# Performance work log

Measured on AMD Instinct MI355X. Metric: run time of the kernel, lower is better.

Reference implementation:

```python
import jax, jax.numpy as jnp
import numpy as np

B, C, H, W = 8, 64, 64, 64
CQ = C // 8  # query/key channels


def setup_inputs() -> dict:
    key = jax.random.key(0)
    ks = jax.random.split(key, 7)
    s = 0.05
    return {
        "x": jax.random.normal(ks[0], (B, C, H, W), jnp.float32),
        "wq": jax.random.normal(ks[1], (CQ, C), jnp.float32) * s,
        "bq": jnp.zeros((CQ,), jnp.float32),
        "wk": jax.random.normal(ks[2], (CQ, C), jnp.float32) * s,
        "bk": jnp.zeros((CQ,), jnp.float32),
        "wv": jax.random.normal(ks[3], (C, C), jnp.float32) * s,
        "bv": jnp.zeros((C,), jnp.float32),
    }


def reference(x, wq, bq, wk, bk, wv, bv):
    b, c, h, w = x.shape
    n = h * w
    xf = x.reshape(b, c, n)                       # [B, C, N]
    # 1x1 convs == per-pixel linear over channels
    q = jnp.einsum('oc,bcn->bon', wq, xf) + bq[None, :, None]   # [B, CQ, N]
    k = jnp.einsum('oc,bcn->bon', wk, xf) + bk[None, :, None]   # [B, CQ, N]
    v = jnp.einsum('oc,bcn->bon', wv, xf) + bv[None, :, None]   # [B, C, N]
    # energy[b, i, j] = q[b, :, i] . k[b, :, j]  (unscaled)
    energy = jnp.einsum('bci,bcj->bij', q, k)     # [B, N, N]
    attention = jax.nn.softmax(energy, axis=-1)   # softmax over j
    # out[b, c, i] = sum_j v[b, c, j] * attention[b, i, j]
    out = jnp.einsum('bcj,bij->bci', v, attention)
    return out.reshape(b, c, h, w)
```

## Files before the change

### kernel.cpp

```cpp
#include <hip/hip_runtime.h>
#include <hip/hip_bf16.h>


#define B_   8
#define C_   64
#define N_   4096
#define LOG2E 1.44269504088896340736f

typedef short bf16x8 __attribute__((ext_vector_type(8)));
typedef float f32x4  __attribute__((ext_vector_type(4)));
typedef unsigned int uint32;

#if __has_builtin(__builtin_amdgcn_exp2f)
#define EXP2(x) __builtin_amdgcn_exp2f(x)
#else
#define EXP2(x) __expf((x) * 0.69314718055994530942f)
#endif

__device__ __forceinline__ unsigned short f2bf_rn(float f) {
    union { __hip_bfloat16 h; unsigned short u; } cv;
    cv.h = __float2bfloat16(f);
    return cv.u;
}
__device__ __forceinline__ uint32 pk_rn(float lo, float hi) {
    return (uint32)f2bf_rn(lo) | ((uint32)f2bf_rn(hi) << 16);
}
__device__ __forceinline__ uint32 pack_rtz(float lo, float hi) {
    return __builtin_amdgcn_perm(__float_as_uint(hi), __float_as_uint(lo), 0x07060302);
}

__global__ __launch_bounds__(256) void prep_kernel(
    const float* __restrict__ x,
    const float* __restrict__ wq, const float* __restrict__ bq,
    const float* __restrict__ wk, const float* __restrict__ bk,
    unsigned short* __restrict__ Qh, unsigned short* __restrict__ Kh,
    unsigned short* __restrict__ Xb)
{
    __shared__ float Xs[C_][64];
    __shared__ float Wqk[16][C_];
    __shared__ float Bqk[16];

    const int t  = threadIdx.x;
    const int b  = blockIdx.x >> 6;
    const int p0 = (blockIdx.x & 63) << 6;

    for (int i = t; i < 1024; i += 256) {
        int o = i >> 6;
        Wqk[o][i & 63] = (o < 8) ? wq[i] * LOG2E : wk[i - 512];
    }
    if (t < 16) Bqk[t] = (t < 8) ? bq[t] * LOG2E : bk[t - 8];

    for (int i = t; i < 2048; i += 256) {
        int c = i >> 5, p2 = (i & 31) << 1;
        const float* xp = x + ((size_t)b * C_ + c) * N_ + p0 + p2;
        float2 v = *(const float2*)xp;
        Xs[c][p2] = v.x; Xs[c][p2 + 1] = v.y;
        *(uint32*)(Xb + ((size_t)b * C_ + c) * N_ + p0 + p2) = pk_rn(v.x, v.y);
    }
    __syncthreads();

    const int pix = t & 63, grp = t >> 6;
    float a[4];
    #pragma unroll
    for (int r = 0; r < 4; ++r) a[r] = Bqk[grp * 4 + r];
    for (int c = 0; c < C_; ++c) {
        float xv = Xs[c][pix];
        #pragma unroll
        for (int r = 0; r < 4; ++r) a[r] += Wqk[grp * 4 + r][c] * xv;
    }
    #pragma unroll
    for (int r = 0; r < 4; ++r) {
        int o = grp * 4 + r;
        unsigned short hv = f2bf_rn(a[r]);
        if (o < 8) Qh[((size_t)b * N_ + p0 + pix) * 8 + o] = hv;
        else       Kh[((size_t)b * N_ + p0 + pix) * 8 + (o - 8)] = hv;
    }
}

__global__ __launch_bounds__(256) void attn_mfma3_kernel(
    const unsigned short* __restrict__ Qh,
    const unsigned short* __restrict__ Kh,
    const unsigned short* __restrict__ Xb,
    const float* __restrict__ wv, const float* __restrict__ bv,
    float* __restrict__ out)
{
    __shared__ __align__(16) char smem[66560];

    const int t    = threadIdx.x;
    const int w    = t >> 6;
    const int lane = t & 63;
    const int l16  = lane & 15;
    const int qd   = lane >> 4;
    const int b    = blockIdx.x >> 6;
    const int i0   = (blockIdx.x & 63) << 6;

    const bf16x8 z8 = {};
    const f32x4  zf = {};

    bf16x8 qf[4];
    #pragma unroll
    for (int qt = 0; qt < 4; ++qt) {
        qf[qt] = z8;
        if (qd == 0)
            qf[qt] = *(const bf16x8*)(Qh + ((size_t)b * N_ + i0 + qt * 16 + l16) * 8);
    }

    const unsigned short* Kp = Kh + ((size_t)b * N_ + w * 1024) * 8;
    const unsigned short* Xp = Xb + (size_t)b * C_ * N_ + w * 1024;

    f32x4 acc[4][4];
    #pragma unroll
    for (int ct = 0; ct < 4; ++ct)
        #pragma unroll
        for (int qt = 0; qt < 4; ++qt) acc[ct][qt] = zf;
    float dsum[4] = {0.f, 0.f, 0.f, 0.f};

    const int swz   = (l16 & 3) << 2;
    const int wbase = w * 4096 + l16 * 64;
    int woff[2];
    #pragma unroll
    for (int jt = 0; jt < 2; ++jt) woff[jt] = ((jt * 8 + qd * 2) ^ swz) << 2;
    const int roff = ((qd * 4) ^ swz) << 2;

    bf16x8 kf[2][2], xf[2][4];
    #pragma unroll
    for (int jt = 0; jt < 2; ++jt) {
        kf[0][jt] = z8;
        if (qd == 0) kf[0][jt] = *(const bf16x8*)(Kp + (jt * 16 + l16) * 8);
    }
    #pragma unroll
    for (int ct = 0; ct < 4; ++ct)
        xf[0][ct] = *(const bf16x8*)(Xp + (size_t)(ct * 16 + l16) * N_ + qd * 8);

    #pragma unroll 2
    for (int s = 0; s < 32; ++s) {
        const int cur = s & 1, nxt = cur ^ 1;
        const int jb = s * 32;

        f32x4 sf[2][4];
        #pragma unroll
        for (int jt = 0; jt < 2; ++jt)
            #pragma unroll
            for (int qt = 0; qt < 4; ++qt)
                sf[jt][qt] = __builtin_amdgcn_mfma_f32_16x16x32_bf16(kf[cur][jt], qf[qt], zf, 0, 0, 0);

        if (s < 31) {
            #pragma unroll
            for (int jt = 0; jt < 2; ++jt) {
                bf16x8 nk = z8;
                if (qd == 0) nk = *(const bf16x8*)(Kp + (size_t)(jb + 32 + jt * 16 + l16) * 8);
                kf[nxt][jt] = nk;
            }
            #pragma unroll
            for (int ct = 0; ct < 4; ++ct)
                xf[nxt][ct] = *(const bf16x8*)(Xp + (size_t)(ct * 16 + l16) * N_ + jb + 32 + qd * 8);
        }

        #pragma unroll
        for (int jt = 0; jt < 2; ++jt)
            #pragma unroll
            for (int qt = 0; qt < 4; ++qt) {
                float e0 = EXP2(sf[jt][qt][0]);
                float e1 = EXP2(sf[jt][qt][1]);
                float e2 = EXP2(sf[jt][qt][2]);
                float e3 = EXP2(sf[jt][qt][3]);
                dsum[qt] += (e0 + e1) + (e2 + e3);
                uint2 u;
                u.x = pack_rtz(e0, e1);
                u.y = pack_rtz(e2, e3);
                *(uint2*)(smem + wbase + qt * 1024 + woff[jt]) = u;
            }

        #pragma unroll
        for (int qt = 0; qt < 4; ++qt) {
            bf16x8 pb = *(const bf16x8*)(smem + wbase + qt * 1024 + roff);
            #pragma unroll
            for (int ct = 0; ct < 4; ++ct)
                acc[ct][qt] = __builtin_amdgcn_mfma_f32_16x16x32_bf16(xf[cur][ct], pb, acc[ct][qt], 0, 0, 0);
        }
    }

    #pragma unroll
    for (int qt = 0; qt < 4; ++qt) {
        float v = dsum[qt];
        v += __shfl_xor(v, 16, 64);
        v += __shfl_xor(v, 32, 64);
        if (qd == 0) *(float*)(smem + 65536 + (w * 64 + qt * 16 + l16) * 4) = v;
    }
    if (w > 0) {
        char* rb = smem + 16384 + (w - 1) * 16384;
        #pragma unroll
        for (int ct = 0; ct < 4; ++ct)
            #pragma unroll
            for (int qt = 0; qt < 4; ++qt)
                *(f32x4*)(rb + (ct * 4 + qt) * 1024 + lane * 16) = acc[ct][qt];
    }
    __syncthreads();

    if (w == 0) {
        #pragma unroll
        for (int rr = 0; rr < 3; ++rr)
            #pragma unroll
            for (int ct = 0; ct < 4; ++ct)
                #pragma unroll
                for (int qt = 0; qt < 4; ++qt) {
                    f32x4 p = *(const f32x4*)(smem + 16384 + rr * 16384 + (ct * 4 + qt) * 1024 + lane * 16);
                    acc[ct][qt] += p;
                }
        float* Or = (float*)(smem + 16384);
        #pragma unroll
        for (int ct = 0; ct < 4; ++ct)
            #pragma unroll
            for (int qt = 0; qt < 4; ++qt)
                #pragma unroll
                for (int r = 0; r < 4; ++r)
                    Or[(ct * 16 + qd * 4 + r) * 64 + qt * 16 + l16] = acc[ct][qt][r];
    } else {
        float* Wvs = (float*)smem;
        for (int i = t - 64; i < 4096; i += 192) Wvs[i] = wv[i];
    }
    __syncthreads();

    const int q = t & 63, grp = t >> 6;
    const float* Wvs = (const float*)smem;
    const float* Or  = (const float*)(smem + 16384);
    const float* Dn  = (const float*)(smem + 65536);
    const float inv = 1.0f / (Dn[q] + Dn[64 + q] + Dn[128 + q] + Dn[192 + q]);
    float o[16];
    #pragma unroll
    for (int r = 0; r < 16; ++r) o[r] = 0.f;
    for (int k = 0; k < 64; ++k) {
        float ov = Or[k * 64 + q];
        #pragma unroll
        for (int r = 0; r < 16; ++r)
            o[r] += Wvs[(grp * 16 + r) * 64 + k] * ov;
    }
    #pragma unroll
    for (int r = 0; r < 16; ++r)
        out[((size_t)b * C_ + grp * 16 + r) * N_ + i0 + q] = o[r] * inv + bv[grp * 16 + r];
}

__global__ __launch_bounds__(256) void attn_fused_fallback(
    const float* __restrict__ x,
    const float* __restrict__ wq, const float* __restrict__ bq,
    const float* __restrict__ wk, const float* __restrict__ bk,
    const float* __restrict__ wv, const float* __restrict__ bv,
    float* __restrict__ out)
{
    __shared__ float Qs[64][8];
    __shared__ float Ks[8][64];
    __shared__ float Vs[64][C_];
    __shared__ float Ws[64][64 + 1];
    __shared__ float Xs[C_ * 64];
    __shared__ float Wks[8][C_];
    __shared__ float Wvs[C_][C_ + 1];

    const int t     = threadIdx.x;
    const int b     = blockIdx.x / (N_ / 64);
    const int i0    = (blockIdx.x % (N_ / 64)) * 64;
    const int jlane = t & 63;
    const int wgrp  = t >> 6;

    for (int l = t; l < 8 * C_;  l += 256) Wks[l >> 6][l & 63] = wk[l];
    for (int l = t; l < C_ * C_; l += 256) Wvs[l >> 6][l & 63] = wv[l];
    for (int l = t; l < C_ * 64; l += 256)
        Xs[(l >> 6) * 64 + (l & 63)] = x[((size_t)b * C_ + (l >> 6)) * N_ + i0 + (l & 63)];
    __syncthreads();
    {
        int qi = jlane;
        #pragma unroll
        for (int r = 0; r < 2; ++r) {
            int cc = wgrp * 2 + r;
            float a = bq[cc];
            for (int c = 0; c < C_; ++c) a += wq[cc * C_ + c] * Xs[c * 64 + qi];
            Qs[qi][cc] = a;
        }
    }
    __syncthreads();

    const int qi2 = t >> 2;
    const int cb  = (t & 3) << 4;
    float accv[16];
    #pragma unroll
    for (int r = 0; r < 16; ++r) accv[r] = 0.f;
    float denom = 0.f;

    for (int j0 = 0; j0 < N_; j0 += 64) {
        for (int l = t; l < C_ * 64; l += 256)
            Xs[(l >> 6) * 64 + (l & 63)] = x[((size_t)b * C_ + (l >> 6)) * N_ + j0 + (l & 63)];
        __syncthreads();
        {
            int j = jlane;
            #pragma unroll
            for (int r = 0; r < 2; ++r) {
                int cc = wgrp * 2 + r;
                float a = bk[cc];
                for (int c = 0; c < C_; ++c) a += Wks[cc][c] * Xs[c * 64 + j];
                Ks[cc][j] = a;
            }
        }
        {
            int vc = jlane;
            #pragma unroll 2
            for (int r = 0; r < 16; ++r) {
                int j = wgrp * 16 + r;
                float a = bv[vc];
                for (int c = 0; c < C_; ++c) a += Wvs[vc][c] * Xs[c * 64 + j];
                Vs[j][vc] = a;
            }
        }
        __syncthreads();
        {
            float kreg[8];
            #pragma unroll
            for (int cc = 0; cc < 8; ++cc) kreg[cc] = Ks[cc][jlane];
            #pragma unroll 4
            for (int r = 0; r < 16; ++r) {
                int qi = wgrp * 16 + r;
                float e = 0.f;
                #pragma unroll
                for (int cc = 0; cc < 8; ++cc) e += Qs[qi][cc] * kreg[cc];
                Ws[qi][jlane] = __expf(e);
            }
        }
        __syncthreads();
        #pragma unroll 4
        for (int j = 0; j < 64; ++j) {
            float wv2 = Ws[qi2][j];
            denom += wv2;
            const float4* vrow = (const float4*)(&Vs[j][cb]);
            float4 v0 = vrow[0], v1 = vrow[1], v2 = vrow[2], v3 = vrow[3];
            accv[0]  += wv2 * v0.x; accv[1]  += wv2 * v0.y; accv[2]  += wv2 * v0.z; accv[3]  += wv2 * v0.w;
            accv[4]  += wv2 * v1.x; accv[5]  += wv2 * v1.y; accv[6]  += wv2 * v1.z; accv[7]  += wv2 * v1.w;
            accv[8]  += wv2 * v2.x; accv[9]  += wv2 * v2.y; accv[10] += wv2 * v2.z; accv[11] += wv2 * v2.w;
            accv[12] += wv2 * v3.x; accv[13] += wv2 * v3.y; accv[14] += wv2 * v3.z; accv[15] += wv2 * v3.w;
        }
        __syncthreads();
    }

    const float inv = 1.0f / denom;
    #pragma unroll
    for (int r = 0; r < 16; ++r)
        out[((size_t)b * C_ + cb + r) * N_ + i0 + qi2] = accv[r] * inv;
}

extern "C" void kernel_launch(void* const* d_in, const int* in_sizes, int n_in,
                              void* d_out, int out_size, void* d_ws, size_t ws_size,
                              hipStream_t stream)
{
    const float* x  = (const float*)d_in[0];
    const float* wq = (const float*)d_in[1];
    const float* bq = (const float*)d_in[2];
    const float* wk = (const float*)d_in[3];
    const float* bk = (const float*)d_in[4];
    const float* wv = (const float*)d_in[5];
    const float* bv = (const float*)d_in[6];
    float* out = (float*)d_out;

    const size_t nQ = (size_t)B_ * N_ * 8;
    const size_t nX = (size_t)B_ * C_ * N_;
    const size_t needed = (2 * nQ + nX) * sizeof(unsigned short);

    if (ws_size >= needed) {
        unsigned short* Qh = (unsigned short*)d_ws;
        unsigned short* Kh = Qh + nQ;
        unsigned short* Xb = Kh + nQ;
        prep_kernel<<<B_ * (N_ / 64), 256, 0, stream>>>(x, wq, bq, wk, bk, Qh, Kh, Xb);
        attn_mfma3_kernel<<<B_ * (N_ / 64), 256, 0, stream>>>(Qh, Kh, Xb, wv, bv, out);
    } else {
        attn_fused_fallback<<<B_ * (N_ / 64), 256, 0, stream>>>(x, wq, bq, wk, bk, wv, bv, out);
    }
}
```

Baseline: 127.5 us.

## Precompute V projection in prep, use K=16 MFMA for QK, shrink LDS

The value projection (Wv·x + bv) moves into the prep kernel, which now computes Q, K and V with MFMA and stores V in bf16. The attention kernel accumulates P·V directly, so the trailing fp32 Wv matmul and its large LDS staging are gone. Q and K are padded to 16 channels, and the 16x16x16 bf16 MFMA (when the builtin exists) replaces the half-zero 16x16x32 instruction for QK. LDS drops to about 21KB with launch_bounds occupancy 3, at the cost of a serialized multi-round cross-wave reduction, an extra bf16 rounding of V, and removal of the explicit V prefetch.

```diff
diff --git a/kernel.cpp b/kernel.cpp
--- a/kernel.cpp
+++ b/kernel.cpp
@@ -8,6 +8,7 @@
 #define LOG2E 1.44269504088896340736f
 
 typedef short bf16x8 __attribute__((ext_vector_type(8)));
+typedef short bf16x4 __attribute__((ext_vector_type(4)));
 typedef float f32x4  __attribute__((ext_vector_type(4)));
 typedef unsigned int uint32;
 
@@ -15,6 +16,12 @@
 #define EXP2(x) __builtin_amdgcn_exp2f(x)
 #else
 #define EXP2(x) __expf((x) * 0.69314718055994530942f)
+#endif
+
+#if __has_builtin(__builtin_amdgcn_mfma_f32_16x16x16bf16_1k)
+#define HAVE_1K 1
+#else
+#define HAVE_1K 0
 #endif
 
 __device__ __forceinline__ unsigned short f2bf_rn(float f) {
@@ -33,58 +40,82 @@
     const float* __restrict__ x,
     const float* __restrict__ wq, const float* __restrict__ bq,
     const float* __restrict__ wk, const float* __restrict__ bk,
-    unsigned short* __restrict__ Qh, unsigned short* __restrict__ Kh,
-    unsigned short* __restrict__ Xb)
+    const float* __restrict__ wv, const float* __restrict__ bv,
+    unsigned short* __restrict__ Qp, unsigned short* __restrict__ Kp,
+    unsigned short* __restrict__ V)
 {
-    __shared__ float Xs[C_][64];
-    __shared__ float Wqk[16][C_];
-    __shared__ float Bqk[16];
+    __shared__ __align__(16) unsigned short Wb[80 * 72];
+    __shared__ __align__(16) unsigned short xT[64 * 72];
 
     const int t  = threadIdx.x;
     const int b  = blockIdx.x >> 6;
     const int p0 = (blockIdx.x & 63) << 6;
 
-    for (int i = t; i < 1024; i += 256) {
+    for (int i = t; i < 5120; i += 256) {
         int o = i >> 6;
-        Wqk[o][i & 63] = (o < 8) ? wq[i] * LOG2E : wk[i - 512];
-    }
-    if (t < 16) Bqk[t] = (t < 8) ? bq[t] * LOG2E : bk[t - 8];
-
+        float v = (o < 8) ? wq[i] * LOG2E : (o < 16) ? wk[i - 512] : wv[i - 1024];
+        Wb[o * 72 + (i & 63)] = f2bf_rn(v);
+    }
     for (int i = t; i < 2048; i += 256) {
         int c = i >> 5, p2 = (i & 31) << 1;
-        const float* xp = x + ((size_t)b * C_ + c) * N_ + p0 + p2;
-        float2 v = *(const float2*)xp;
-        Xs[c][p2] = v.x; Xs[c][p2 + 1] = v.y;
-        *(uint32*)(Xb + ((size_t)b * C_ + c) * N_ + p0 + p2) = pk_rn(v.x, v.y);
+        float2 v = *(const float2*)(x + ((size_t)b * C_ + c) * N_ + p0 + p2);
+        xT[p2 * 72 + c]       = f2bf_rn(v.x);
+        xT[(p2 + 1) * 72 + c] = f2bf_rn(v.y);
     }
     __syncthreads();
 
-    const int pix = t & 63, grp = t >> 6;
-    float a[4];
-    #pragma unroll
-    for (int r = 0; r < 4; ++r) a[r] = Bqk[grp * 4 + r];
-    for (int c = 0; c < C_; ++c) {
-        float xv = Xs[c][pix];
-        #pragma unroll
-        for (int r = 0; r < 4; ++r) a[r] += Wqk[grp * 4 + r][c] * xv;
-    }
-    #pragma unroll
-    for (int r = 0; r < 4; ++r) {
-        int o = grp * 4 + r;
-        unsigned short hv = f2bf_rn(a[r]);
-        if (o < 8) Qh[((size_t)b * N_ + p0 + pix) * 8 + o] = hv;
-        else       Kh[((size_t)b * N_ + p0 + pix) * 8 + (o - 8)] = hv;
-    }
-}
-
-__global__ __launch_bounds__(256) void attn_mfma3_kernel(
-    const unsigned short* __restrict__ Qh,
-    const unsigned short* __restrict__ Kh,
-    const unsigned short* __restrict__ Xb,
-    const float* __restrict__ wv, const float* __restrict__ bv,
+    const int w = t >> 6, lane = t & 63, l16 = lane & 15, qd = lane >> 4;
+    const f32x4 zf = {};
+
+    bf16x8 bfr[2];
+    #pragma unroll
+    for (int ks = 0; ks < 2; ++ks)
+        bfr[ks] = *(const bf16x8*)(xT + (w * 16 + l16) * 72 + ks * 32 + qd * 8);
+    const int px = p0 + w * 16 + l16;
+
+    {
+        f32x4 acc;
+        #pragma unroll
+        for (int r = 0; r < 4; ++r) {
+            int o = qd * 4 + r;
+            acc[r] = (o < 8) ? bq[o] * LOG2E : bk[o - 8];
+        }
+        bf16x8 af0, af1;
+        af0 = *(const bf16x8*)(Wb + l16 * 72 + qd * 8);
+        af1 = *(const bf16x8*)(Wb + l16 * 72 + 32 + qd * 8);
+        acc = __builtin_amdgcn_mfma_f32_16x16x32_bf16(af0, bfr[0], acc, 0, 0, 0);
+        acc = __builtin_amdgcn_mfma_f32_16x16x32_bf16(af1, bfr[1], acc, 0, 0, 0);
+        uint2 u;
+        u.x = pk_rn(acc[0], acc[1]);
+        u.y = pk_rn(acc[2], acc[3]);
+        unsigned short* base = (qd < 2) ? Qp : Kp;
+        size_t row = ((size_t)b * N_ + px) * 16;
+        *(uint2*)(base + row + (qd & 1) * 4) = u;
+        uint2 z; z.x = 0; z.y = 0;
+        *(uint2*)(base + row + 8 + (qd & 1) * 4) = z;
+    }
+    #pragma unroll
+    for (int mt = 1; mt < 5; ++mt) {
+        const int ch = mt * 16 + qd * 4 - 16;
+        f32x4 acc = {bv[ch], bv[ch + 1], bv[ch + 2], bv[ch + 3]};
+        bf16x8 af0, af1;
+        af0 = *(const bf16x8*)(Wb + (mt * 16 + l16) * 72 + qd * 8);
+        af1 = *(const bf16x8*)(Wb + (mt * 16 + l16) * 72 + 32 + qd * 8);
+        acc = __builtin_amdgcn_mfma_f32_16x16x32_bf16(af0, bfr[0], acc, 0, 0, 0);
+        acc = __builtin_amdgcn_mfma_f32_16x16x32_bf16(af1, bfr[1], acc, 0, 0, 0);
+        #pragma unroll
+        for (int r = 0; r < 4; ++r)
+            V[((size_t)b * C_ + ch + r) * N_ + px] = f2bf_rn(acc[r]);
+    }
+}
+
+__global__ __launch_bounds__(256, 3) void attn_mfma4_kernel(
+    const unsigned short* __restrict__ Qp,
+    const unsigned short* __restrict__ Kp,
+    const unsigned short* __restrict__ V,
     float* __restrict__ out)
 {
-    __shared__ __align__(16) char smem[66560];
+    __shared__ __align__(16) char smem[21504];
 
     const int t    = threadIdx.x;
     const int w    = t >> 6;
@@ -94,150 +125,153 @@
     const int b    = blockIdx.x >> 6;
     const int i0   = (blockIdx.x & 63) << 6;
 
+    const f32x4 zf = {};
     const bf16x8 z8 = {};
-    const f32x4  zf = {};
-
+
+#if HAVE_1K
+    bf16x4 qf[4];
+    #pragma unroll
+    for (int qt = 0; qt < 4; ++qt)
+        qf[qt] = *(const bf16x4*)(Qp + ((size_t)b * N_ + i0 + qt * 16 + l16) * 16 + qd * 4);
+#else
     bf16x8 qf[4];
     #pragma unroll
     for (int qt = 0; qt < 4; ++qt) {
         qf[qt] = z8;
-        if (qd == 0)
-            qf[qt] = *(const bf16x8*)(Qh + ((size_t)b * N_ + i0 + qt * 16 + l16) * 8);
-    }
-
-    const unsigned short* Kp = Kh + ((size_t)b * N_ + w * 1024) * 8;
-    const unsigned short* Xp = Xb + (size_t)b * C_ * N_ + w * 1024;
+        if (qd < 2)
+            qf[qt] = *(const bf16x8*)(Qp + ((size_t)b * N_ + i0 + qt * 16 + l16) * 16 + qd * 8);
+    }
+#endif
+
+    const unsigned short* KpW = Kp + ((size_t)b * N_ + w * 1024) * 16;
+    const unsigned short* Vw  = V + (size_t)b * C_ * N_ + w * 1024;
 
     f32x4 acc[4][4];
     #pragma unroll
-    for (int ct = 0; ct < 4; ++ct)
-        #pragma unroll
-        for (int qt = 0; qt < 4; ++qt) acc[ct][qt] = zf;
+    for (int qt = 0; qt < 4; ++qt)
+        #pragma unroll
+        for (int ct = 0; ct < 4; ++ct) acc[qt][ct] = zf;
     float dsum[4] = {0.f, 0.f, 0.f, 0.f};
 
-    const int swz   = (l16 & 3) << 2;
-    const int wbase = w * 4096 + l16 * 64;
-    int woff[2];
-    #pragma unroll
-    for (int jt = 0; jt < 2; ++jt) woff[jt] = ((jt * 8 + qd * 2) ^ swz) << 2;
-    const int roff = ((qd * 4) ^ swz) << 2;
-
-    bf16x8 kf[2][2], xf[2][4];
+    char* PsW = smem + w * 5120;
+    const int wrbase = l16 * 80 + qd * 8;
+    const int rdbase = l16 * 80 + qd * 16;
+
+#if HAVE_1K
+    bf16x4 kf[2][2];
+    #pragma unroll
+    for (int jt = 0; jt < 2; ++jt)
+        kf[0][jt] = *(const bf16x4*)(KpW + (jt * 16 + l16) * 16 + qd * 4);
+#else
+    bf16x8 kf[2][2];
     #pragma unroll
     for (int jt = 0; jt < 2; ++jt) {
         kf[0][jt] = z8;
-        if (qd == 0) kf[0][jt] = *(const bf16x8*)(Kp + (jt * 16 + l16) * 8);
-    }
-    #pragma unroll
-    for (int ct = 0; ct < 4; ++ct)
-        xf[0][ct] = *(const bf16x8*)(Xp + (size_t)(ct * 16 + l16) * N_ + qd * 8);
-
-    #pragma unroll 2
+        if (qd < 2)
+            kf[0][jt] = *(const bf16x8*)(KpW + (jt * 16 + l16) * 16 + qd * 8);
+    }
+#endif
+
     for (int s = 0; s < 32; ++s) {
         const int cur = s & 1, nxt = cur ^ 1;
         const int jb = s * 32;
 
-        f32x4 sf[2][4];
-        #pragma unroll
-        for (int jt = 0; jt < 2; ++jt)
+        bf16x8 vf[4];
+        #pragma unroll
+        for (int ct = 0; ct < 4; ++ct)
+            vf[ct] = *(const bf16x8*)(Vw + (size_t)(ct * 16 + l16) * N_ + jb + qd * 8);
+
+        if (s < 31) {
+            #pragma unroll
+            for (int jt = 0; jt < 2; ++jt) {
+#if HAVE_1K
+                kf[nxt][jt] = *(const bf16x4*)(KpW + (size_t)(jb + 32 + jt * 16 + l16) * 16 + qd * 4);
+#else
+                kf[nxt][jt] = z8;
+                if (qd < 2)
+                    kf[nxt][jt] = *(const bf16x8*)(KpW + (size_t)(jb + 32 + jt * 16 + l16) * 16 + qd * 8);
+#endif
+            }
+        }
+
+        #pragma unroll
+        for (int jt = 0; jt < 2; ++jt) {
+            f32x4 sf[4];
             #pragma unroll
             for (int qt = 0; qt < 4; ++qt)
-                sf[jt][qt] = __builtin_amdgcn_mfma_f32_16x16x32_bf16(kf[cur][jt], qf[qt], zf, 0, 0, 0);
-
-        if (s < 31) {
-            #pragma unroll
-            for (int jt = 0; jt < 2; ++jt) {
-                bf16x8 nk = z8;
-                if (qd == 0) nk = *(const bf16x8*)(Kp + (size_t)(jb + 32 + jt * 16 + l16) * 8);
-                kf[nxt][jt] = nk;
-            }
-            #pragma unroll
-            for (int ct = 0; ct < 4; ++ct)
-                xf[nxt][ct] = *(const bf16x8*)(Xp + (size_t)(ct * 16 + l16) * N_ + jb + 32 + qd * 8);
-        }
-
-        #pragma unroll
-        for (int jt = 0; jt < 2; ++jt)
+#if HAVE_1K
+                sf[qt] = __builtin_amdgcn_mfma_f32_16x16x16bf16_1k(kf[cur][jt], qf[qt], zf, 0, 0, 0);
+#else
+                sf[qt] = __builtin_amdgcn_mfma_f32_16x16x32_bf16(kf[cur][jt], qf[qt], zf, 0, 0, 0);
+#endif
             #pragma unroll
             for (int qt = 0; qt < 4; ++qt) {
-                float e0 = EXP2(sf[jt][qt][0]);
-                float e1 = EXP2(sf[jt][qt][1]);
-                float e2 = EXP2(sf[jt][qt][2]);
-                float e3 = EXP2(sf[jt][qt][3]);
+                float e0 = EXP2(sf[qt][0]);
+                float e1 = EXP2(sf[qt][1]);
+                float e2 = EXP2(sf[qt][2]);
+                float e3 = EXP2(sf[qt][3]);
                 dsum[qt] += (e0 + e1) + (e2 + e3);
                 uint2 u;
                 u.x = pack_rtz(e0, e1);
                 u.y = pack_rtz(e2, e3);
-                *(uint2*)(smem + wbase + qt * 1024 + woff[jt]) = u;
+                *(uint2*)(PsW + qt * 1280 + wrbase + jt * 32) = u;
             }
+        }
 
         #pragma unroll
         for (int qt = 0; qt < 4; ++qt) {
-            bf16x8 pb = *(const bf16x8*)(smem + wbase + qt * 1024 + roff);
+            bf16x8 pb = *(const bf16x8*)(PsW + qt * 1280 + rdbase);
             #pragma unroll
             for (int ct = 0; ct < 4; ++ct)
-                acc[ct][qt] = __builtin_amdgcn_mfma_f32_16x16x32_bf16(xf[cur][ct], pb, acc[ct][qt], 0, 0, 0);
-        }
-    }
-
+                acc[qt][ct] = __builtin_amdgcn_mfma_f32_16x16x32_bf16(vf[ct], pb, acc[qt][ct], 0, 0, 0);
+        }
+    }
+
+    float* Dn = (float*)(smem + 20480);
     #pragma unroll
     for (int qt = 0; qt < 4; ++qt) {
         float v = dsum[qt];
         v += __shfl_xor(v, 16, 64);
         v += __shfl_xor(v, 32, 64);
-        if (qd == 0) *(float*)(smem + 65536 + (w * 64 + qt * 16 + l16) * 4) = v;
-    }
-    if (w > 0) {
-        char* rb = smem + 16384 + (w - 1) * 16384;
-        #pragma unroll
-        for (int ct = 0; ct < 4; ++ct)
+        if (qd == 0) Dn[w * 64 + qt * 16 + l16] = v;
+    }
+    __syncthreads();
+
+    float* rb = (float*)smem;
+    #pragma unroll
+    for (int rnd = 1; rnd < 4; ++rnd) {
+        if (w == rnd) {
             #pragma unroll
             for (int qt = 0; qt < 4; ++qt)
-                *(f32x4*)(rb + (ct * 4 + qt) * 1024 + lane * 16) = acc[ct][qt];
-    }
-    __syncthreads();
+                #pragma unroll
+                for (int ct = 0; ct < 4; ++ct)
+                    *(f32x4*)(rb + ((qt * 4 + ct) * 64 + lane) * 4) = acc[qt][ct];
+        }
+        __syncthreads();
+        if (w == 0) {
+            #pragma unroll
+            for (int qt = 0; qt < 4; ++qt)
+                #pragma unroll
+                for (int ct = 0; ct < 4; ++ct) {
+                    f32x4 p = *(const f32x4*)(rb + ((qt * 4 + ct) * 64 + lane) * 4);
+                    acc[qt][ct] += p;
+                }
+        }
+        __syncthreads();
+    }
 
     if (w == 0) {
         #pragma unroll
-        for (int rr = 0; rr < 3; ++rr)
+        for (int qt = 0; qt < 4; ++qt) {
+            const int q = qt * 16 + l16;
+            const float inv = 1.0f / (Dn[q] + Dn[64 + q] + Dn[128 + q] + Dn[192 + q]);
             #pragma unroll
             for (int ct = 0; ct < 4; ++ct)
                 #pragma unroll
-                for (int qt = 0; qt < 4; ++qt) {
-                    f32x4 p = *(const f32x4*)(smem + 16384 + rr * 16384 + (ct * 4 + qt) * 1024 + lane * 16);
-                    acc[ct][qt] += p;
-                }
-        float* Or = (float*)(smem + 16384);
-        #pragma unroll
-        for (int ct = 0; ct < 4; ++ct)
-            #pragma unroll
-            for (int qt = 0; qt < 4; ++qt)
-                #pragma unroll
                 for (int r = 0; r < 4; ++r)
-                    Or[(ct * 16 + qd * 4 + r) * 64 + qt * 16 + l16] = acc[ct][qt][r];
-    } else {
-        float* Wvs = (float*)smem;
-        for (int i = t - 64; i < 4096; i += 192) Wvs[i] = wv[i];
-    }
-    __syncthreads();
-
-    const int q = t & 63, grp = t >> 6;
-    const float* Wvs = (const float*)smem;
-    const float* Or  = (const float*)(smem + 16384);
-    const float* Dn  = (const float*)(smem + 65536);
-    const float inv = 1.0f / (Dn[q] + Dn[64 + q] + Dn[128 + q] + Dn[192 + q]);
-    float o[16];
-    #pragma unroll
-    for (int r = 0; r < 16; ++r) o[r] = 0.f;
-    for (int k = 0; k < 64; ++k) {
-        float ov = Or[k * 64 + q];
-        #pragma unroll
-        for (int r = 0; r < 16; ++r)
-            o[r] += Wvs[(grp * 16 + r) * 64 + k] * ov;
-    }
-    #pragma unroll
-    for (int r = 0; r < 16; ++r)
-        out[((size_t)b * C_ + grp * 16 + r) * N_ + i0 + q] = o[r] * inv + bv[grp * 16 + r];
+                    out[((size_t)b * C_ + ct * 16 + qd * 4 + r) * N_ + i0 + q] = acc[qt][ct][r] * inv;
+        }
+    }
 }
 
 __global__ __launch_bounds__(256) void attn_fused_fallback(
@@ -357,16 +391,17 @@
     const float* bv = (const float*)d_in[6];
     float* out = (float*)d_out;
 
-    const size_t nQ = (size_t)B_ * N_ * 8;
-    const size_t nX = (size_t)B_ * C_ * N_;
-    const size_t needed = (2 * nQ + nX) * sizeof(unsigned short);
+    const size_t nQ = (size_t)B_ * N_ * 16;
+    const size_t nV = (size_t)B_ * C_ * N_;
+    const size_t needed = (2 * nQ + nV) * sizeof(unsigned short);
 
     if (ws_size >= needed) {
-        unsigned short* Qh = (unsigned short*)d_ws;
-        unsigned short* Kh = Qh + nQ;
-        unsigned short* Xb = Kh + nQ;
-        prep_kernel<<<B_ * (N_ / 64), 256, 0, stream>>>(x, wq, bq, wk, bk, Qh, Kh, Xb);
-        attn_mfma3_kernel<<<B_ * (N_ / 64), 256, 0, stream>>>(Qh, Kh, Xb, wv, bv, out);
+        unsigned short* Qp = (unsigned short*)d_ws;
+        unsigned short* Kp = Qp + nQ;
+        unsigned short* Vb = Kp + nQ;
+        prep_kernel<<<B_ * (N_ / 64), 256, 0, stream>>>(x, wq, bq, wk, bk, wv, bv,
+                                                        Qp, Kp, Vb);
+        attn_mfma4_kernel<<<B_ * (N_ / 64), 256, 0, stream>>>(Qp, Kp, Vb, out);
     } else {
         attn_fused_fallback<<<B_ * (N_ / 64), 256, 0, stream>>>(x, wq, bq, wk, bk, wv, bv, out);
     }
```

Measured after the change: 210.2 us. 64.9% more time.
